# Performance work log

Measured on AMD Instinct MI355X. Metric: run time of the kernel, lower is better.

Reference implementation:

```python
import jax, jax.numpy as jnp
import numpy as np

M = 2048
K = 512


def setup_inputs() -> dict:
    key = jax.random.key(0)
    k1, k2, k3, k4, k5 = jax.random.split(key, 5)
    inputs = jax.random.normal(k1, (16384, M), dtype=jnp.float32)
    # MyLinear(m, k): weight [k, m], bias [k] (torch Linear convention)
    s1 = 1.0 / np.sqrt(M)
    s2 = 1.0 / np.sqrt(K)
    W1 = jax.random.uniform(k2, (K, M), jnp.float32, -s1, s1)
    b1 = jax.random.uniform(k3, (K,), jnp.float32, -s1, s1)
    W2 = jax.random.uniform(k4, (M, K), jnp.float32, -s2, s2)
    b2 = jax.random.uniform(k5, (M,), jnp.float32, -s2, s2)
    return {"inputs": inputs, "W1": W1, "b1": b1, "W2": W2, "b2": b2}


def reference(inputs, W1, b1, W2, b2):
    # Original loops per sample; math is identical to one batched chain:
    # hidden = x @ W1^T + b1 ; out = hidden @ W2^T + b2 (no nonlinearity)
    hidden = jnp.einsum("bm,km->bk", inputs, W1) + b1  # [B, K]
    out = jnp.einsum("bk,mk->bm", hidden, W2) + b2     # [B, M]
    return out
```

## Files before the change

### kernel.cpp

```cpp
#include <hip/hip_runtime.h>
#include <hip/hip_bf16.h>
#include <stdint.h>


typedef short bf16x8 __attribute__((ext_vector_type(8)));
typedef float f32x4 __attribute__((ext_vector_type(4)));

static __device__ __forceinline__ unsigned short f32_to_bf16_rne(float f) {
    unsigned int u = __float_as_uint(f);
    u += 0x7fffu + ((u >> 16) & 1u);
    return (unsigned short)(u >> 16);
}

__global__ void cast_bf16_all(const float* __restrict__ x,
                              unsigned short* __restrict__ xo, int nx4,
                              const float* __restrict__ w1,
                              unsigned short* __restrict__ w1o,
                              const float* __restrict__ w2,
                              unsigned short* __restrict__ w2o, int nw4) {
    const int total = nx4 + 2 * nw4;
    const int stride = gridDim.x * blockDim.x;
    for (int i = blockIdx.x * blockDim.x + threadIdx.x; i < total; i += stride) {
        const float* in;
        unsigned short* out;
        int j;
        if (i < nx4) {
            in = x; out = xo; j = i;
        } else if (i < nx4 + nw4) {
            in = w1; out = w1o; j = i - nx4;
        } else {
            in = w2; out = w2o; j = i - nx4 - nw4;
        }
        float4 v = ((const float4*)in)[j];
        ushort4 o;
        o.x = f32_to_bf16_rne(v.x);
        o.y = f32_to_bf16_rne(v.y);
        o.z = f32_to_bf16_rne(v.z);
        o.w = f32_to_bf16_rne(v.w);
        ((ushort4*)out)[j] = o;
    }
}

#define GLOAD_LDS16(gsrc, ldst)                                              \
    __builtin_amdgcn_global_load_lds(                                        \
        (const __attribute__((address_space(1))) void*)(gsrc),               \
        (__attribute__((address_space(3))) void*)(ldst), 16, 0, 0)

__global__ __launch_bounds__(256)
void gemm1_bf(const unsigned short* __restrict__ A,
              const unsigned short* __restrict__ Bt,
              const float* __restrict__ bias,
              unsigned short* __restrict__ H) {
    constexpr int N = 512, Kd = 2048, BK = 64, NSTEP = Kd / BK;

    __shared__ __align__(16) unsigned short ldsA[128 * BK];
    __shared__ __align__(16) unsigned short ldsB[128 * BK];

    const int tid  = threadIdx.x;
    const int lane = tid & 63;
    const int wid  = tid >> 6;
    const int wr   = wid >> 1;
    const int wc   = wid & 1;

    const int bid = blockIdx.x;
    const int swz = ((bid & 7) << 6) + (bid >> 3);
    const int bm  = swz >> 2;
    const int bn  = swz & 3;
    const int brow = bm << 7;
    const int bcol = bn << 7;

    const int lrow = lane & 15;
    const int ku   = lane >> 4;
    const int rx   = lrow & 7;

    const int srow = tid >> 3;
    const int sgu  = (tid & 7) ^ (srow & 7);

    f32x4 acc[4][4] = {};

    auto stage = [&](int k0) {
#pragma unroll
        for (int i = 0; i < 4; ++i) {
            const int row = i * 32 + srow;
            const char* sa =
                (const char*)(A + (size_t)(brow + row) * Kd + k0) + (sgu << 4);
            const char* sb =
                (const char*)(Bt + (size_t)(bcol + row) * Kd + k0) + (sgu << 4);
            GLOAD_LDS16(sa, (char*)ldsA + i * 4096 + tid * 16);
            GLOAD_LDS16(sb, (char*)ldsB + i * 4096 + tid * 16);
        }
    };
    auto compute = [&]() {
#pragma unroll
        for (int kk = 0; kk < 2; ++kk) {
            const int un = ((ku + (kk << 2)) ^ rx) << 4;
            bf16x8 a[4], b[4];
#pragma unroll
            for (int m = 0; m < 4; ++m)
                a[m] = *(const bf16x8*)((const char*)ldsA +
                       ((wr << 6) + (m << 4) + lrow) * 128 + un);
#pragma unroll
            for (int n = 0; n < 4; ++n)
                b[n] = *(const bf16x8*)((const char*)ldsB +
                       ((wc << 6) + (n << 4) + lrow) * 128 + un);
#pragma unroll
            for (int m = 0; m < 4; ++m)
#pragma unroll
                for (int n = 0; n < 4; ++n)
                    acc[m][n] = __builtin_amdgcn_mfma_f32_16x16x32_bf16(
                        a[m], b[n], acc[m][n], 0, 0, 0);
        }
    };

    stage(0);
    __syncthreads();

#pragma unroll 1
    for (int t = 0; t < NSTEP; ++t) {
        compute();
        if (t + 1 < NSTEP) {
            __syncthreads();
            stage((t + 1) * BK);
            __syncthreads();
        }
    }

    const int r0 = (lane >> 4) << 2;
#pragma unroll
    for (int n = 0; n < 4; ++n) {
        const int col = bcol + (wc << 6) + (n << 4) + lrow;
        const float bb = bias[col];
#pragma unroll
        for (int m = 0; m < 4; ++m)
#pragma unroll
            for (int j = 0; j < 4; ++j) {
                const int row = brow + (wr << 6) + (m << 4) + r0 + j;
                H[(size_t)row * N + col] = f32_to_bf16_rne(acc[m][n][j] + bb);
            }
    }
}

__global__ __launch_bounds__(256)
void gemm2(const unsigned short* __restrict__ A,
           const unsigned short* __restrict__ Bt,
           const float* __restrict__ bias,
           float* __restrict__ C) {
    constexpr int N = 2048, Kd = 512, BK = 64, NSTEP = Kd / BK;

    __shared__ __align__(16) unsigned short ldsA[128 * BK];
    __shared__ __align__(16) unsigned short ldsB[128 * BK];

    const int tid  = threadIdx.x;
    const int lane = tid & 63;
    const int wid  = tid >> 6;
    const int wr   = wid >> 1;
    const int wc   = wid & 1;

    const int bid = blockIdx.x;
    const int swz = ((bid & 7) << 8) + (bid >> 3);
    const int bn  = swz & 15;
    const int bm  = swz >> 4;
    const int brow = bm << 7;
    const int bcol = bn << 7;

    const int lrow = lane & 15;
    const int ku   = lane >> 4;
    const int rx   = lrow & 7;

    const int srow = tid >> 3;
    const int sgu  = (tid & 7) ^ (srow & 7);

    f32x4 acc[4][4] = {};

    auto stage = [&](int k0) {
#pragma unroll
        for (int i = 0; i < 4; ++i) {
            const int row = i * 32 + srow;
            const char* sa =
                (const char*)(A + (size_t)(brow + row) * Kd + k0) + (sgu << 4);
            const char* sb =
                (const char*)(Bt + (size_t)(bcol + row) * Kd + k0) + (sgu << 4);
            GLOAD_LDS16(sa, (char*)ldsA + i * 4096 + tid * 16);
            GLOAD_LDS16(sb, (char*)ldsB + i * 4096 + tid * 16);
        }
    };
    auto compute = [&]() {
#pragma unroll
        for (int kk = 0; kk < 2; ++kk) {
            const int un = ((ku + (kk << 2)) ^ rx) << 4;
            bf16x8 a[4], b[4];
#pragma unroll
            for (int m = 0; m < 4; ++m)
                a[m] = *(const bf16x8*)((const char*)ldsA +
                       ((wr << 6) + (m << 4) + lrow) * 128 + un);
#pragma unroll
            for (int n = 0; n < 4; ++n)
                b[n] = *(const bf16x8*)((const char*)ldsB +
                       ((wc << 6) + (n << 4) + lrow) * 128 + un);
#pragma unroll
            for (int m = 0; m < 4; ++m)
#pragma unroll
                for (int n = 0; n < 4; ++n)
                    acc[m][n] = __builtin_amdgcn_mfma_f32_16x16x32_bf16(
                        a[m], b[n], acc[m][n], 0, 0, 0);
        }
    };

    stage(0);
    __syncthreads();

    for (int t = 0; t < NSTEP; ++t) {
        compute();
        if (t + 1 < NSTEP) {
            __syncthreads();
            stage((t + 1) * BK);
            __syncthreads();
        }
    }

    const int r0 = (lane >> 4) << 2;
#pragma unroll
    for (int n = 0; n < 4; ++n) {
        const int col = bcol + (wc << 6) + (n << 4) + lrow;
        const float bb = bias[col];
#pragma unroll
        for (int m = 0; m < 4; ++m)
#pragma unroll
            for (int j = 0; j < 4; ++j) {
                const int row = brow + (wr << 6) + (m << 4) + r0 + j;
                C[(size_t)row * N + col] = acc[m][n][j] + bb;
            }
    }
}

extern "C" void kernel_launch(void* const* d_in, const int* in_sizes, int n_in,
                              void* d_out, int out_size, void* d_ws, size_t ws_size,
                              hipStream_t stream) {
    const float* X  = (const float*)d_in[0];
    const float* W1 = (const float*)d_in[1];
    const float* b1 = (const float*)d_in[2];
    const float* W2 = (const float*)d_in[3];
    const float* b2 = (const float*)d_in[4];

    const int B = 16384, M = 2048, Kd = 512;

    char* ws = (char*)d_ws;
    unsigned short* W1bf = (unsigned short*)ws;
    unsigned short* W2bf = W1bf + (size_t)Kd * M;
    unsigned short* Hbf  = W2bf + (size_t)M * Kd;
    unsigned short* Xbf  = Hbf + (size_t)B * Kd;

    const int nx4 = B * M / 4;
    const int nw4 = Kd * M / 4;

    cast_bf16_all<<<4096, 256, 0, stream>>>(X, Xbf, nx4, W1, W1bf, W2, W2bf,
                                            nw4);

    gemm1_bf<<<(B / 128) * (Kd / 128), 256, 0, stream>>>(Xbf, W1bf, b1, Hbf);
    gemm2<<<(B / 128) * (M / 128), 256, 0, stream>>>(Hbf, W2bf, b2,
                                                     (float*)d_out);
}
```

Baseline: 136.1 us.

## Split-K gemm1 four ways with atomic fp32 accumulation and separate bias/cast pass

gemm1 originally launched only 512 blocks, each walking the full K=2048. It now splits K into four chunks, giving 2048 blocks that accumulate into a zeroed fp32 buffer with atomics. A new combineH kernel adds the bias and converts the result to bf16 for gemm2, and the cast kernel also zeroes the accumulator. This raises occupancy on the GPU at the cost of an extra fp32 buffer round-trip, atomic traffic, an extra launch, and non-deterministic summation order.

Measured after the change: 227.8 us. 1.67x slower.

```diff
diff --git a/kernel.cpp b/kernel.cpp
--- a/kernel.cpp
+++ b/kernel.cpp
@@ -12,15 +12,21 @@
     return (unsigned short)(u >> 16);
 }
 
-__global__ void cast_bf16_all(const float* __restrict__ x,
-                              unsigned short* __restrict__ xo, int nx4,
-                              const float* __restrict__ w1,
-                              unsigned short* __restrict__ w1o,
-                              const float* __restrict__ w2,
-                              unsigned short* __restrict__ w2o, int nw4) {
-    const int total = nx4 + 2 * nw4;
+__global__ void cast_zero(const float* __restrict__ x,
+                          unsigned short* __restrict__ xo, int nx4,
+                          const float* __restrict__ w1,
+                          unsigned short* __restrict__ w1o,
+                          const float* __restrict__ w2,
+                          unsigned short* __restrict__ w2o, int nw4,
+                          float* __restrict__ hf, int nh4) {
+    const int total = nx4 + 2 * nw4 + nh4;
     const int stride = gridDim.x * blockDim.x;
     for (int i = blockIdx.x * blockDim.x + threadIdx.x; i < total; i += stride) {
+        if (i >= nx4 + 2 * nw4) {
+            float4 z = {0.f, 0.f, 0.f, 0.f};
+            ((float4*)hf)[i - nx4 - 2 * nw4] = z;
+            continue;
+        }
         const float* in;
         unsigned short* out;
         int j;
@@ -41,17 +47,34 @@
     }
 }
 
+__global__ void combineH(const float* __restrict__ Hf,
+                         const float* __restrict__ b1,
+                         unsigned short* __restrict__ Hbf, int n4) {
+    const int stride = gridDim.x * blockDim.x;
+    for (int i = blockIdx.x * blockDim.x + threadIdx.x; i < n4; i += stride) {
+        float4 v = ((const float4*)Hf)[i];
+        const int c = (i << 2) & 511;
+        float4 bb = *(const float4*)(b1 + c);
+        ushort4 o;
+        o.x = f32_to_bf16_rne(v.x + bb.x);
+        o.y = f32_to_bf16_rne(v.y + bb.y);
+        o.z = f32_to_bf16_rne(v.z + bb.z);
+        o.w = f32_to_bf16_rne(v.w + bb.w);
+        ((ushort4*)Hbf)[i] = o;
+    }
+}
+
 #define GLOAD_LDS16(gsrc, ldst)                                              \
     __builtin_amdgcn_global_load_lds(                                        \
         (const __attribute__((address_space(1))) void*)(gsrc),               \
         (__attribute__((address_space(3))) void*)(ldst), 16, 0, 0)
 
 __global__ __launch_bounds__(256)
-void gemm1_bf(const unsigned short* __restrict__ A,
-              const unsigned short* __restrict__ Bt,
-              const float* __restrict__ bias,
-              unsigned short* __restrict__ H) {
-    constexpr int N = 512, Kd = 2048, BK = 64, NSTEP = Kd / BK;
+void gemm1_splitk(const unsigned short* __restrict__ A,
+                  const unsigned short* __restrict__ Bt,
+                  float* __restrict__ Hf) {
+    constexpr int N = 512, K = 2048, BK = 64, KSPLIT = 512;
+    constexpr int NSTEP = KSPLIT / BK;
 
     __shared__ __align__(16) unsigned short ldsA[128 * BK];
     __shared__ __align__(16) unsigned short ldsB[128 * BK];
@@ -63,9 +86,105 @@
     const int wc   = wid & 1;
 
     const int bid = blockIdx.x;
-    const int swz = ((bid & 7) << 6) + (bid >> 3);
-    const int bm  = swz >> 2;
-    const int bn  = swz & 3;
+    const int swz = ((bid & 7) << 8) + (bid >> 3);
+    const int kv   = swz >> 9;
+    const int tile = swz & 511;
+    const int bm  = tile >> 2;
+    const int bn  = tile & 3;
+    const int brow = bm << 7;
+    const int bcol = bn << 7;
+    const int kbase = kv * KSPLIT;
+
+    const int lrow = lane & 15;
+    const int ku   = lane >> 4;
+    const int rx   = lrow & 7;
+
+    const int srow = tid >> 3;
+    const int sgu  = (tid & 7) ^ (srow & 7);
+
+    f32x4 acc[4][4] = {};
+
+    auto stage = [&](int k0) {
+#pragma unroll
+        for (int i = 0; i < 4; ++i) {
+            const int row = i * 32 + srow;
+            const char* sa =
+                (const char*)(A + (size_t)(brow + row) * K + k0) + (sgu << 4);
+            const char* sb =
+                (const char*)(Bt + (size_t)(bcol + row) * K + k0) + (sgu << 4);
+            GLOAD_LDS16(sa, (char*)ldsA + i * 4096 + tid * 16);
+            GLOAD_LDS16(sb, (char*)ldsB + i * 4096 + tid * 16);
+        }
+    };
+    auto compute = [&]() {
+#pragma unroll
+        for (int kk = 0; kk < 2; ++kk) {
+            const int un = ((ku + (kk << 2)) ^ rx) << 4;
+            bf16x8 a[4], b[4];
+#pragma unroll
+            for (int m = 0; m < 4; ++m)
+                a[m] = *(const bf16x8*)((const char*)ldsA +
+                       ((wr << 6) + (m << 4) + lrow) * 128 + un);
+#pragma unroll
+            for (int n = 0; n < 4; ++n)
+                b[n] = *(const bf16x8*)((const char*)ldsB +
+                       ((wc << 6) + (n << 4) + lrow) * 128 + un);
+#pragma unroll
+            for (int m = 0; m < 4; ++m)
+#pragma unroll
+                for (int n = 0; n < 4; ++n)
+                    acc[m][n] = __builtin_amdgcn_mfma_f32_16x16x32_bf16(
+                        a[m], b[n], acc[m][n], 0, 0, 0);
+        }
+    };
+
+    stage(kbase);
+    __syncthreads();
+
+#pragma unroll 1
+    for (int t = 0; t < NSTEP; ++t) {
+        compute();
+        if (t + 1 < NSTEP) {
+            __syncthreads();
+            stage(kbase + (t + 1) * BK);
+            __syncthreads();
+        }
+    }
+
+    const int r0 = (lane >> 4) << 2;
+#pragma unroll
+    for (int n = 0; n < 4; ++n) {
+        const int col = bcol + (wc << 6) + (n << 4) + lrow;
+#pragma unroll
+        for (int m = 0; m < 4; ++m)
+#pragma unroll
+            for (int j = 0; j < 4; ++j) {
+                const int row = brow + (wr << 6) + (m << 4) + r0 + j;
+                unsafeAtomicAdd(&Hf[(size_t)row * N + col], acc[m][n][j]);
+            }
+    }
+}
+
+__global__ __launch_bounds__(256)
+void gemm2(const unsigned short* __restrict__ A,
+           const unsigned short* __restrict__ Bt,
+           const float* __restrict__ bias,
+           float* __restrict__ C) {
+    constexpr int N = 2048, Kd = 512, BK = 64, NSTEP = Kd / BK;
+
+    __shared__ __align__(16) unsigned short ldsA[128 * BK];
+    __shared__ __align__(16) unsigned short ldsB[128 * BK];
+
+    const int tid  = threadIdx.x;
+    const int lane = tid & 63;
+    const int wid  = tid >> 6;
+    const int wr   = wid >> 1;
+    const int wc   = wid & 1;
+
+    const int bid = blockIdx.x;
+    const int swz = ((bid & 7) << 8) + (bid >> 3);
+    const int bn  = swz & 15;
+    const int bm  = swz >> 4;
     const int brow = bm << 7;
     const int bcol = bn << 7;
 
@@ -115,100 +234,6 @@
     stage(0);
     __syncthreads();
 
-#pragma unroll 1
-    for (int t = 0; t < NSTEP; ++t) {
-        compute();
-        if (t + 1 < NSTEP) {
-            __syncthreads();
-            stage((t + 1) * BK);
-            __syncthreads();
-        }
-    }
-
-    const int r0 = (lane >> 4) << 2;
-#pragma unroll
-    for (int n = 0; n < 4; ++n) {
-        const int col = bcol + (wc << 6) + (n << 4) + lrow;
-        const float bb = bias[col];
-#pragma unroll
-        for (int m = 0; m < 4; ++m)
-#pragma unroll
-            for (int j = 0; j < 4; ++j) {
-                const int row = brow + (wr << 6) + (m << 4) + r0 + j;
-                H[(size_t)row * N + col] = f32_to_bf16_rne(acc[m][n][j] + bb);
-            }
-    }
-}
-
-__global__ __launch_bounds__(256)
-void gemm2(const unsigned short* __restrict__ A,
-           const unsigned short* __restrict__ Bt,
-           const float* __restrict__ bias,
-           float* __restrict__ C) {
-    constexpr int N = 2048, Kd = 512, BK = 64, NSTEP = Kd / BK;
-
-    __shared__ __align__(16) unsigned short ldsA[128 * BK];
-    __shared__ __align__(16) unsigned short ldsB[128 * BK];
-
-    const int tid  = threadIdx.x;
-    const int lane = tid & 63;
-    const int wid  = tid >> 6;
-    const int wr   = wid >> 1;
-    const int wc   = wid & 1;
-
-    const int bid = blockIdx.x;
-    const int swz = ((bid & 7) << 8) + (bid >> 3);
-    const int bn  = swz & 15;
-    const int bm  = swz >> 4;
-    const int brow = bm << 7;
-    const int bcol = bn << 7;
-
-    const int lrow = lane & 15;
-    const int ku   = lane >> 4;
-    const int rx   = lrow & 7;
-
-    const int srow = tid >> 3;
-    const int sgu  = (tid & 7) ^ (srow & 7);
-
-    f32x4 acc[4][4] = {};
-
-    auto stage = [&](int k0) {
-#pragma unroll
-        for (int i = 0; i < 4; ++i) {
-            const int row = i * 32 + srow;
-            const char* sa =
-                (const char*)(A + (size_t)(brow + row) * Kd + k0) + (sgu << 4);
-            const char* sb =
-                (const char*)(Bt + (size_t)(bcol + row) * Kd + k0) + (sgu << 4);
-            GLOAD_LDS16(sa, (char*)ldsA + i * 4096 + tid * 16);
-            GLOAD_LDS16(sb, (char*)ldsB + i * 4096 + tid * 16);
-        }
-    };
-    auto compute = [&]() {
-#pragma unroll
-        for (int kk = 0; kk < 2; ++kk) {
-            const int un = ((ku + (kk << 2)) ^ rx) << 4;
-            bf16x8 a[4], b[4];
-#pragma unroll
-            for (int m = 0; m < 4; ++m)
-                a[m] = *(const bf16x8*)((const char*)ldsA +
-                       ((wr << 6) + (m << 4) + lrow) * 128 + un);
-#pragma unroll
-            for (int n = 0; n < 4; ++n)
-                b[n] = *(const bf16x8*)((const char*)ldsB +
-                       ((wc << 6) + (n << 4) + lrow) * 128 + un);
-#pragma unroll
-            for (int m = 0; m < 4; ++m)
-#pragma unroll
-                for (int n = 0; n < 4; ++n)
-                    acc[m][n] = __builtin_amdgcn_mfma_f32_16x16x32_bf16(
-                        a[m], b[n], acc[m][n], 0, 0, 0);
-        }
-    };
-
-    stage(0);
-    __syncthreads();
-
     for (int t = 0; t < NSTEP; ++t) {
         compute();
         if (t + 1 < NSTEP) {
@@ -249,14 +274,19 @@
     unsigned short* W2bf = W1bf + (size_t)Kd * M;
     unsigned short* Hbf  = W2bf + (size_t)M * Kd;
     unsigned short* Xbf  = Hbf + (size_t)B * Kd;
+    float*          Hf   = (float*)(Xbf + (size_t)B * M);
 
     const int nx4 = B * M / 4;
     const int nw4 = Kd * M / 4;
-
-    cast_bf16_all<<<4096, 256, 0, stream>>>(X, Xbf, nx4, W1, W1bf, W2, W2bf,
-                                            nw4);
-
-    gemm1_bf<<<(B / 128) * (Kd / 128), 256, 0, stream>>>(Xbf, W1bf, b1, Hbf);
+    const int nh4 = B * Kd / 4;
+
+    cast_zero<<<4096, 256, 0, stream>>>(X, Xbf, nx4, W1, W1bf, W2, W2bf, nw4,
+                                        Hf, nh4);
+
+    gemm1_splitk<<<4 * (B / 128) * (Kd / 128), 256, 0, stream>>>(Xbf, W1bf, Hf);
+
+    combineH<<<2048, 256, 0, stream>>>(Hf, b1, Hbf, nh4);
+
     gemm2<<<(B / 128) * (M / 128), 256, 0, stream>>>(Hbf, W2bf, b2,
                                                      (float*)d_out);
 }
```
